# Kernel optimization log

Measured on AMD Instinct MI355X. Metric: run time of the kernel, lower is better.

Reference implementation:

```python
import jax, jax.numpy as jnp
import numpy as np

D = 64        # in_out_dim
M = 512       # hidden_dim
N = 4096      # batch
R = 10        # rank of quadratic term A (min(10, d+1))
ALPHA0 = 1.0  # alpha[0]
H = 1.0       # ResNet step h = 1/(nTh-1), nTh=2


def antideriv_tanh(x):
    # log(2*cosh(x)), numerically stable antiderivative of tanh
    ax = jnp.abs(x)
    return ax + jnp.log1p(jnp.exp(-2.0 * ax))


def setup_inputs() -> dict:
    key = jax.random.key(0)
    ks = jax.random.split(key, 10)
    f32 = jnp.float32
    return {
        "x":   jax.random.normal(ks[0], (N, D), f32),
        "t":   jax.random.uniform(ks[1], (), f32),
        "K0":  jax.random.normal(ks[2], (M, D + 1), f32) * (1.0 / np.sqrt(D + 1)),
        "b0":  jax.random.normal(ks[3], (M,), f32) * 0.1,
        "K1":  jax.random.normal(ks[4], (M, M), f32) * (1.0 / np.sqrt(M)),
        "b1":  jax.random.normal(ks[5], (M,), f32) * 0.1,
        "w":   jax.random.normal(ks[6], (M,), f32) * (1.0 / np.sqrt(M)),
        "A":   jax.random.normal(ks[7], (R, D + 1), f32) * (1.0 / np.sqrt(D + 1)),
        "c_w": jax.random.normal(ks[8], (D + 1,), f32) * 0.1,
        "c_b": jax.random.normal(ks[9], (), f32) * 0.1,
    }


def _tr_hess(s, K0, b0, K1, b1, w, A, c_w):
    # s: [N, d+1]; analytic gradient + Hessian trace of the OT-Flow potential.
    d = s.shape[1] - 1
    symA = A.T @ A                                   # [d+1, d+1]

    # forward through ResNet (nTh=2 -> one residual layer)
    opening = s @ K0.T + b0                          # [N, m]
    u0 = antideriv_tanh(opening)                     # [N, m]
    lin1 = u0 @ K1.T + b1                            # [N, m]

    tanh_open = jnp.tanh(opening)
    tanh_lin1 = jnp.tanh(lin1)

    # backward z-chain for the gradient
    z1 = w + H * (tanh_lin1 * w) @ K1                # [N, m]
    z0 = (tanh_open * z1) @ K0                       # [N, d+1]
    grad = z0 + s @ symA + c_w                       # [N, d+1]

    # trace of Hessian w.r.t. the first d coordinates
    Kopen = K0[:, :d]                                # [m, d]
    dt_open = 1.0 - tanh_open ** 2
    trH = (dt_open * z1) @ jnp.sum(Kopen ** 2, axis=1)          # [N]
    Jac = tanh_open[:, :, None] * Kopen[None]                    # [N, m, d]
    KJ = jnp.einsum('ij,njk->nik', K1, Jac)                      # [N, m, d]
    dt_lin1 = 1.0 - tanh_lin1 ** 2
    t1 = jnp.einsum('nj,njk->n', dt_lin1 * w, KJ ** 2)           # [N]
    trH = trH + H * t1 + jnp.trace(symA[:d, :d])
    return grad, trH


def reference(x, t, K0, b0, K1, b1, w, A, c_w, c_b):
    n = x.shape[0]
    s = jnp.concatenate([x, jnp.ones((n, 1), x.dtype) * t], axis=1)  # pad time
    gradPhi, trH = _tr_hess(s, K0, b0, K1, b1, w, A, c_w)
    dPhi_dx = gradPhi[:, :D]                         # [N, d]
    dPhi_dt = gradPhi[:, D:D + 1]                    # [N, 1]
    dz_dt = -(1.0 / ALPHA0) * dPhi_dx
    dlogp_dt = -(1.0 / ALPHA0) * trH[:, None]
    cost_L_dt = 0.5 * jnp.sum(dz_dt ** 2, axis=1, keepdims=True)
    cost_HJB_dt = jnp.abs(-dPhi_dt + ALPHA0 * cost_L_dt)
    return (dz_dt, dlogp_dt, cost_L_dt, cost_HJB_dt)
```

## Files before the change

### kernel.cpp

```cpp
#include <hip/hip_runtime.h>
#include <stdint.h>

#define D_  64
#define DP1 65
#define M_  512
#define N_  4096

typedef float f32x4 __attribute__((ext_vector_type(4)));
typedef _Float16 h8 __attribute__((ext_vector_type(8)));

__global__ void prepk(const float* __restrict__ A, const float* __restrict__ K0,
                      const float* __restrict__ K1, const float* __restrict__ x,
                      const float* __restrict__ tptr, const float* __restrict__ b0,
                      float* symA, float* sumK2,
                      _Float16* K1h, _Float16* K1Th, _Float16* K0Th,
                      _Float16* u0h, _Float16* ah, float* trH0){
  __shared__ float shm[2*64*66];
  int b = blockIdx.x;
  int t = threadIdx.x;
  if (b == 0){
    for (int idx = t; idx < DP1*DP1; idx += 256){
      int e = idx / DP1, d = idx % DP1;
      float s = 0.f;
      for (int r = 0; r < 10; ++r) s += A[r*DP1+e]*A[r*DP1+d];
      symA[idx] = s;
    }
    for (int m = t; m < M_; m += 256){
      float s = 0.f;
      for (int k = 0; k < D_; ++k){ float v = K0[m*DP1+k]; s += v*v; }
      sumK2[m] = s;
    }
  } else if (b < 65){
    int bb = b - 1;
    int r0 = (bb>>3)*64, c0 = (bb&7)*64;
    float* tile = shm;
    for (int it = 0; it < 16; ++it){
      int lin = it*256 + t;
      int r = lin >> 6, c = lin & 63;
      float v = K1[(r0+r)*M_ + c0+c];
      tile[r*65+c] = v;
      K1h[(r0+r)*M_ + c0+c] = (_Float16)v;
    }
    __syncthreads();
    for (int it = 0; it < 16; ++it){
      int lin = it*256 + t;
      int r = lin >> 6, c = lin & 63;
      K1Th[(c0+r)*M_ + (r0+c)] = (_Float16)tile[c*65+r];
    }
  } else if (b < 225){
    int idx = (b-65)*256 + t;
    if (idx < 80*M_){
      int d = idx / M_, i = idx % M_;
      float v = (d < DP1) ? K0[i*DP1 + d] : 0.f;
      K0Th[idx] = (_Float16)v;
    }
  } else {
    int bb = b - 225;
    int n0 = (bb & 63)*64, m0 = (bb >> 6)*64;
    float* sS = shm;
    float* sK = shm + 64*66;
    float tval = tptr[0];
    for (int it = 0; it < 17; ++it){
      int lin = it*256 + t;
      if (lin < 64*65){
        int r = lin/65, c = lin%65;
        sS[r*66+c] = (c < 64) ? x[(n0+r)*64 + c] : tval;
        sK[r*66+c] = K0[(m0+r)*DP1 + c];
      }
    }
    __syncthreads();
    int tn = (t>>4)*4, tm = (t&15)*4;
    float acc[4][4] = {};
    for (int e = 0; e < DP1; ++e){
      float sv[4], kv[4];
      for (int i=0;i<4;++i){ sv[i]=sS[(tn+i)*66+e]; kv[i]=sK[(tm+i)*66+e]; }
      for (int i=0;i<4;++i) for(int j=0;j<4;++j) acc[i][j] += sv[i]*kv[j];
    }
    for (int i=0;i<4;++i) for(int j=0;j<4;++j){
      int n = n0+tn+i, m = m0+tm+j;
      float o = acc[i][j] + b0[m];
      float a = tanhf(o);
      float ax = fabsf(o);
      float u0 = ax + log1pf(expf(-2.f*ax));
      u0h[n*M_+m] = (_Float16)u0;
      ah[n*M_+m]  = (_Float16)a;
    }
    if (m0 == 0 && t < 64) trH0[n0+t] = 0.f;
  }
}

template<int MODE>
__launch_bounds__(256, 4)
__global__ void gemm512(const _Float16* __restrict__ Ah, const _Float16* __restrict__ Wh,
                        const float* __restrict__ bias, const float* __restrict__ w,
                        const _Float16* __restrict__ ah, const float* __restrict__ sumK2,
                        _Float16* out0, _Float16* out1, float* trH0){
  int n0 = blockIdx.x*64, i0 = blockIdx.y*64;
  int t = threadIdx.x;
  int wv = t>>6, l = t&63;
  int r15 = l & 15;
  int krow = (l>>4)*8;
  const _Float16* abase = Ah + (size_t)(n0 + wv*16 + r15)*M_ + krow;
  const _Float16* wb0 = Wh + (size_t)(i0 +  0 + r15)*M_ + krow;
  const _Float16* wb1 = Wh + (size_t)(i0 + 16 + r15)*M_ + krow;
  const _Float16* wb2 = Wh + (size_t)(i0 + 32 + r15)*M_ + krow;
  const _Float16* wb3 = Wh + (size_t)(i0 + 48 + r15)*M_ + krow;
  f32x4 zero = {0.f,0.f,0.f,0.f};
  f32x4 acc[4]; for (int k=0;k<4;++k) acc[k]=zero;
  h8 af_c = *(const h8*)(abase);
  h8 bf_c0 = *(const h8*)(wb0);
  h8 bf_c1 = *(const h8*)(wb1);
  h8 bf_c2 = *(const h8*)(wb2);
  h8 bf_c3 = *(const h8*)(wb3);
  #pragma unroll
  for (int ii = 0; ii < 16; ++ii){
    const int j0 = ii*32;
    h8 af_n, bf_n0, bf_n1, bf_n2, bf_n3;
    if (ii < 15){
      af_n  = *(const h8*)(abase + j0 + 32);
      bf_n0 = *(const h8*)(wb0 + j0 + 32);
      bf_n1 = *(const h8*)(wb1 + j0 + 32);
      bf_n2 = *(const h8*)(wb2 + j0 + 32);
      bf_n3 = *(const h8*)(wb3 + j0 + 32);
    }
    acc[0] = __builtin_amdgcn_mfma_f32_16x16x32_f16(af_c, bf_c0, acc[0], 0, 0, 0);
    acc[1] = __builtin_amdgcn_mfma_f32_16x16x32_f16(af_c, bf_c1, acc[1], 0, 0, 0);
    acc[2] = __builtin_amdgcn_mfma_f32_16x16x32_f16(af_c, bf_c2, acc[2], 0, 0, 0);
    acc[3] = __builtin_amdgcn_mfma_f32_16x16x32_f16(af_c, bf_c3, acc[3], 0, 0, 0);
    if (ii < 15){
      af_c = af_n; bf_c0 = bf_n0; bf_c1 = bf_n1; bf_c2 = bf_n2; bf_c3 = bf_n3;
    }
  }
  if (MODE == 0){
    for (int kt=0;kt<4;++kt) for (int r=0;r<4;++r){
      int n = n0+wv*16+(l>>4)*4+r;
      int i = i0+kt*16+r15;
      float v = acc[kt][r] + bias[i];
      float tl = tanhf(v);
      out0[n*M_+i] = (_Float16)(tl*w[i]);
      out1[n*M_+i] = (_Float16)((1.f-tl*tl)*w[i]);
    }
  } else {
    for (int r=0;r<4;++r){
      int n = n0+wv*16+(l>>4)*4+r;
      float rowpart = 0.f;
      for (int kt=0;kt<4;++kt){
        int i = i0+kt*16+r15;
        float z1 = acc[kt][r] + w[i];
        float a = (float)ah[n*M_+i];
        out0[n*M_+i] = (_Float16)(a*z1);
        rowpart += (1.f-a*a)*z1*sumK2[i];
      }
      for (int m=1;m<16;m<<=1) rowpart += __shfl_xor(rowpart, m);
      if (r15==0) atomicAdd(&trH0[n], rowpart);
    }
  }
}

__launch_bounds__(256, 4)
__global__ void gemmz0(const _Float16* __restrict__ az1h, const _Float16* __restrict__ K0Th,
                       float* z0){
  int n0 = blockIdx.x*64;
  int t = threadIdx.x, wv = t>>6, l = t&63;
  int r15 = l & 15;
  int krow = (l>>4)*8;
  const _Float16* abase = az1h + (size_t)(n0 + wv*16 + r15)*M_ + krow;
  const _Float16* kb0 = K0Th + (size_t)( 0 + r15)*M_ + krow;
  const _Float16* kb1 = K0Th + (size_t)(16 + r15)*M_ + krow;
  const _Float16* kb2 = K0Th + (size_t)(32 + r15)*M_ + krow;
  const _Float16* kb3 = K0Th + (size_t)(48 + r15)*M_ + krow;
  const _Float16* kb4 = K0Th + (size_t)(64 + r15)*M_ + krow;
  f32x4 zero = {0.f,0.f,0.f,0.f};
  f32x4 acc[5]; for (int k=0;k<5;++k) acc[k]=zero;
  h8 af_c = *(const h8*)(abase);
  h8 b0c = *(const h8*)(kb0);
  h8 b1c = *(const h8*)(kb1);
  h8 b2c = *(const h8*)(kb2);
  h8 b3c = *(const h8*)(kb3);
  h8 b4c = *(const h8*)(kb4);
  #pragma unroll
  for (int ii = 0; ii < 16; ++ii){
    const int j0 = ii*32;
    h8 af_n, b0n, b1n, b2n, b3n, b4n;
    if (ii < 15){
      af_n = *(const h8*)(abase + j0 + 32);
      b0n = *(const h8*)(kb0 + j0 + 32);
      b1n = *(const h8*)(kb1 + j0 + 32);
      b2n = *(const h8*)(kb2 + j0 + 32);
      b3n = *(const h8*)(kb3 + j0 + 32);
      b4n = *(const h8*)(kb4 + j0 + 32);
    }
    acc[0] = __builtin_amdgcn_mfma_f32_16x16x32_f16(af_c, b0c, acc[0], 0, 0, 0);
    acc[1] = __builtin_amdgcn_mfma_f32_16x16x32_f16(af_c, b1c, acc[1], 0, 0, 0);
    acc[2] = __builtin_amdgcn_mfma_f32_16x16x32_f16(af_c, b2c, acc[2], 0, 0, 0);
    acc[3] = __builtin_amdgcn_mfma_f32_16x16x32_f16(af_c, b3c, acc[3], 0, 0, 0);
    acc[4] = __builtin_amdgcn_mfma_f32_16x16x32_f16(af_c, b4c, acc[4], 0, 0, 0);
    if (ii < 15){
      af_c = af_n; b0c = b0n; b1c = b1n; b2c = b2n; b3c = b3n; b4c = b4n;
    }
  }
  for (int dt=0; dt<5; ++dt) for (int r=0;r<4;++r){
    int n = n0+wv*16+(l>>4)*4+r;
    int d = dt*16+r15;
    z0[n*80+d] = acc[dt][r];
  }
}

__launch_bounds__(256, 2)
__global__ void kjk11(const _Float16* __restrict__ K1h, const _Float16* __restrict__ K0Th,
                      const _Float16* __restrict__ ah, const _Float16* __restrict__ ch,
                      float* trH0){
  __shared__ _Float16 sK1[64*512];
  __shared__ _Float16 sAv[8*512];
  int t = threadIdx.x;
  int n0 = blockIdx.x*8;
  int i0 = blockIdx.y*64;
  int wv = t>>6, l = t&63;
  int c15 = l & 15, g = l>>4;
  h8 kf[16];
  {
    const _Float16* kfp = K0Th + (size_t)(wv*16 + c15)*M_ + g*8;
    #pragma unroll
    for (int tt = 0; tt < 16; ++tt) kf[tt] = *(const h8*)(kfp + tt*32);
  }
  #pragma unroll
  for (int it = 0; it < 16; ++it){
    int r = it*4 + wv;
    const _Float16* src = K1h + (size_t)(i0 + r)*M_ + ((l ^ (r & 7))*8);
    __builtin_amdgcn_global_load_lds(
        (const __attribute__((address_space(1))) void*)src,
        (__attribute__((address_space(3))) void*)(&sK1[r*512]), 16, 0, 0);
  }
  #pragma unroll
  for (int it = 0; it < 2; ++it){
    int cc = it*256 + t;
    int s = cc >> 6, c = cc & 63;
    *(h8*)(&sAv[s*512 + c*8]) = *(const h8*)(ah + (size_t)(n0+s)*M_ + c*8);
  }
  __syncthreads();
  f32x4 zero = {0.f,0.f,0.f,0.f};
  f32x4 acc[4][8];
  #pragma unroll
  for (int tt=0;tt<4;++tt)
    #pragma unroll
    for (int s=0;s<8;++s) acc[tt][s]=zero;
  #pragma unroll
  for (int step = 0; step < 16; ++step){
    int p0 = (((step*4 + g) ^ (c15 & 7))*8);
    h8 bf0 = *(const h8*)(&sK1[(     c15)*512 + p0]);
    h8 bf1 = *(const h8*)(&sK1[(16 + c15)*512 + p0]);
    h8 bf2 = *(const h8*)(&sK1[(32 + c15)*512 + p0]);
    h8 bf3 = *(const h8*)(&sK1[(48 + c15)*512 + p0]);
    int aoff = step*32 + g*8;
    h8 k = kf[step];
    #pragma unroll
    for (int s = 0; s < 8; ++s){
      h8 av = *(const h8*)(&sAv[s*512 + aoff]);
      h8 ap = k*av;
      acc[0][s] = __builtin_amdgcn_mfma_f32_16x16x32_f16(ap, bf0, acc[0][s], 0, 0, 0);
      acc[1][s] = __builtin_amdgcn_mfma_f32_16x16x32_f16(ap, bf1, acc[1][s], 0, 0, 0);
      acc[2][s] = __builtin_amdgcn_mfma_f32_16x16x32_f16(ap, bf2, acc[2][s], 0, 0, 0);
      acc[3][s] = __builtin_amdgcn_mfma_f32_16x16x32_f16(ap, bf3, acc[3][s], 0, 0, 0);
    }
  }
  #pragma unroll
  for (int s = 0; s < 8; ++s){
    float part = 0.f;
    #pragma unroll
    for (int tt = 0; tt < 4; ++tt){
      float ci = (float)ch[(size_t)(n0+s)*M_ + i0 + tt*16 + c15];
      f32x4 a = acc[tt][s];
      part += ci*(a[0]*a[0] + a[1]*a[1] + a[2]*a[2] + a[3]*a[3]);
    }
    for (int m=32;m>=1;m>>=1) part += __shfl_xor(part, m);
    if (l == 0) atomicAdd(&trH0[n0+s], part);
  }
}

__global__ void finalk(const float* __restrict__ x, const float* __restrict__ tptr,
                       const float* __restrict__ symA, const float* __restrict__ c_w,
                       const float* __restrict__ z0, const float* __restrict__ trH0,
                       float* out){
  __shared__ float sA[DP1*DP1];
  int t = threadIdx.x;
  for (int i = t; i < DP1*DP1; i += 256) sA[i] = symA[i];
  __syncthreads();
  int wv = t>>6, l = t&63;
  int n = blockIdx.x*4 + wv;
  float tval = tptr[0];
  float sv = x[n*64 + l];
  float acc = z0[n*80 + l] + c_w[l];
  for (int e = 0; e < 64; ++e){
    float se = __shfl(sv, e);
    acc += se * sA[l*DP1 + e];
  }
  acc += tval * sA[l*DP1 + 64];
  float trd = sA[l*66];
  for (int m=32;m>=1;m>>=1) trd += __shfl_xor(trd, m);
  float g64 = sv * sA[64*DP1 + l];
  for (int m=32;m>=1;m>>=1) g64 += __shfl_xor(g64, m);
  g64 += tval*sA[64*DP1+64] + z0[n*80+64] + c_w[64];
  float dz = -acc;
  out[n*64 + l] = dz;
  float q = dz*dz;
  for (int m=32;m>=1;m>>=1) q += __shfl_xor(q, m);
  float costL = 0.5f*q;
  if (l == 0){
    out[N_*64 + n]        = -(trH0[n] + trd);
    out[N_*64 + N_ + n]   = costL;
    out[N_*64 + 2*N_ + n] = fabsf(-g64 + costL);
  }
}

extern "C" void kernel_launch(void* const* d_in, const int* in_sizes, int n_in,
                              void* d_out, int out_size, void* d_ws, size_t ws_size,
                              hipStream_t stream){
  const float* x   = (const float*)d_in[0];
  const float* tp  = (const float*)d_in[1];
  const float* K0  = (const float*)d_in[2];
  const float* b0  = (const float*)d_in[3];
  const float* K1  = (const float*)d_in[4];
  const float* b1  = (const float*)d_in[5];
  const float* w   = (const float*)d_in[6];
  const float* A   = (const float*)d_in[7];
  const float* c_w = (const float*)d_in[8];
  float* out = (float*)d_out;

  char* ws = (char*)d_ws;
  size_t off = 0;
  auto alloc = [&](size_t bytes)->void*{
    void* p = ws + off; off += bytes; off = (off + 255) & ~(size_t)255; return p;
  };
  _Float16* K1h   = (_Float16*)alloc(512*512*2);
  _Float16* K1Th  = (_Float16*)alloc(512*512*2);
  _Float16* K0Th  = (_Float16*)alloc(80*512*2);
  float* symA     = (float*)alloc(DP1*DP1*4);
  float* sumK2    = (float*)alloc(512*4);
  _Float16* u0h   = (_Float16*)alloc((size_t)N_*M_*2);
  _Float16* ah    = (_Float16*)alloc((size_t)N_*M_*2);
  _Float16* tl1wh = (_Float16*)alloc((size_t)N_*M_*2);
  _Float16* ch    = (_Float16*)alloc((size_t)N_*M_*2);
  _Float16* az1h  = (_Float16*)alloc((size_t)N_*M_*2);
  float* z0       = (float*)alloc((size_t)N_*80*4);
  float* trH0     = (float*)alloc(N_*4);

  prepk<<<737, 256, 0, stream>>>(A, K0, K1, x, tp, b0, symA, sumK2,
                                 K1h, K1Th, K0Th, u0h, ah, trH0);
  gemm512<0><<<dim3(N_/64, M_/64), 256, 0, stream>>>(u0h, K1h, b1, w, nullptr, nullptr,
                                                     tl1wh, ch, nullptr);
  gemm512<1><<<dim3(N_/64, M_/64), 256, 0, stream>>>(tl1wh, K1Th, nullptr, w, ah, sumK2,
                                                     az1h, nullptr, trH0);
  gemmz0<<<N_/64, 256, 0, stream>>>(az1h, K0Th, z0);
  kjk11<<<dim3(N_/8, 8), 256, 0, stream>>>(K1h, K0Th, ah, ch, trH0);
  finalk<<<N_/4, 256, 0, stream>>>(x, tp, symA, c_w, z0, trH0, out);
}
```

Before: 221.9 us.

## Split gemmz0 over K into four partial sums and raise MFMA priority in kjk

The z0 GEMM (N x 512 -> 80) now splits its K dimension across four blocks in a new grid y-dimension. Each block writes a partial result to its own slice of a buffer, and finalk adds the four slices. This takes the grid from 64 blocks to 256 so more CUs are busy, in exchange for extra partial-sum traffic and four loads per element in finalk. Separately, the kjk kernel raises wave priority around its MFMA inner loop with s_setprio, to favour issuing matrix instructions.

Measured after the change: 217.6 us. About the same (-1.9%).

```diff
diff --git a/kernel.cpp b/kernel.cpp
--- a/kernel.cpp
+++ b/kernel.cpp
@@ -159,11 +159,12 @@
 
 __launch_bounds__(256, 4)
 __global__ void gemmz0(const _Float16* __restrict__ az1h, const _Float16* __restrict__ K0Th,
-                       float* z0){
+                       float* z0p){
   int n0 = blockIdx.x*64;
+  int q  = blockIdx.y;
   int t = threadIdx.x, wv = t>>6, l = t&63;
   int r15 = l & 15;
-  int krow = (l>>4)*8;
+  int krow = q*128 + (l>>4)*8;
   const _Float16* abase = az1h + (size_t)(n0 + wv*16 + r15)*M_ + krow;
   const _Float16* kb0 = K0Th + (size_t)( 0 + r15)*M_ + krow;
   const _Float16* kb1 = K0Th + (size_t)(16 + r15)*M_ + krow;
@@ -172,42 +173,31 @@
   const _Float16* kb4 = K0Th + (size_t)(64 + r15)*M_ + krow;
   f32x4 zero = {0.f,0.f,0.f,0.f};
   f32x4 acc[5]; for (int k=0;k<5;++k) acc[k]=zero;
-  h8 af_c = *(const h8*)(abase);
-  h8 b0c = *(const h8*)(kb0);
-  h8 b1c = *(const h8*)(kb1);
-  h8 b2c = *(const h8*)(kb2);
-  h8 b3c = *(const h8*)(kb3);
-  h8 b4c = *(const h8*)(kb4);
-  #pragma unroll
-  for (int ii = 0; ii < 16; ++ii){
+  #pragma unroll
+  for (int ii = 0; ii < 4; ++ii){
     const int j0 = ii*32;
-    h8 af_n, b0n, b1n, b2n, b3n, b4n;
-    if (ii < 15){
-      af_n = *(const h8*)(abase + j0 + 32);
-      b0n = *(const h8*)(kb0 + j0 + 32);
-      b1n = *(const h8*)(kb1 + j0 + 32);
-      b2n = *(const h8*)(kb2 + j0 + 32);
-      b3n = *(const h8*)(kb3 + j0 + 32);
-      b4n = *(const h8*)(kb4 + j0 + 32);
-    }
-    acc[0] = __builtin_amdgcn_mfma_f32_16x16x32_f16(af_c, b0c, acc[0], 0, 0, 0);
-    acc[1] = __builtin_amdgcn_mfma_f32_16x16x32_f16(af_c, b1c, acc[1], 0, 0, 0);
-    acc[2] = __builtin_amdgcn_mfma_f32_16x16x32_f16(af_c, b2c, acc[2], 0, 0, 0);
-    acc[3] = __builtin_amdgcn_mfma_f32_16x16x32_f16(af_c, b3c, acc[3], 0, 0, 0);
-    acc[4] = __builtin_amdgcn_mfma_f32_16x16x32_f16(af_c, b4c, acc[4], 0, 0, 0);
-    if (ii < 15){
-      af_c = af_n; b0c = b0n; b1c = b1n; b2c = b2n; b3c = b3n; b4c = b4n;
-    }
-  }
+    h8 af = *(const h8*)(abase + j0);
+    h8 b0c = *(const h8*)(kb0 + j0);
+    h8 b1c = *(const h8*)(kb1 + j0);
+    h8 b2c = *(const h8*)(kb2 + j0);
+    h8 b3c = *(const h8*)(kb3 + j0);
+    h8 b4c = *(const h8*)(kb4 + j0);
+    acc[0] = __builtin_amdgcn_mfma_f32_16x16x32_f16(af, b0c, acc[0], 0, 0, 0);
+    acc[1] = __builtin_amdgcn_mfma_f32_16x16x32_f16(af, b1c, acc[1], 0, 0, 0);
+    acc[2] = __builtin_amdgcn_mfma_f32_16x16x32_f16(af, b2c, acc[2], 0, 0, 0);
+    acc[3] = __builtin_amdgcn_mfma_f32_16x16x32_f16(af, b3c, acc[3], 0, 0, 0);
+    acc[4] = __builtin_amdgcn_mfma_f32_16x16x32_f16(af, b4c, acc[4], 0, 0, 0);
+  }
+  float* zp = z0p + (size_t)q*N_*80;
   for (int dt=0; dt<5; ++dt) for (int r=0;r<4;++r){
     int n = n0+wv*16+(l>>4)*4+r;
     int d = dt*16+r15;
-    z0[n*80+d] = acc[dt][r];
+    zp[n*80+d] = acc[dt][r];
   }
 }
 
 __launch_bounds__(256, 2)
-__global__ void kjk11(const _Float16* __restrict__ K1h, const _Float16* __restrict__ K0Th,
+__global__ void kjk12(const _Float16* __restrict__ K1h, const _Float16* __restrict__ K0Th,
                       const _Float16* __restrict__ ah, const _Float16* __restrict__ ch,
                       float* trH0){
   __shared__ _Float16 sK1[64*512];
@@ -253,6 +243,7 @@
     h8 bf3 = *(const h8*)(&sK1[(48 + c15)*512 + p0]);
     int aoff = step*32 + g*8;
     h8 k = kf[step];
+    __builtin_amdgcn_s_setprio(1);
     #pragma unroll
     for (int s = 0; s < 8; ++s){
       h8 av = *(const h8*)(&sAv[s*512 + aoff]);
@@ -262,6 +253,7 @@
       acc[2][s] = __builtin_amdgcn_mfma_f32_16x16x32_f16(ap, bf2, acc[2][s], 0, 0, 0);
       acc[3][s] = __builtin_amdgcn_mfma_f32_16x16x32_f16(ap, bf3, acc[3][s], 0, 0, 0);
     }
+    __builtin_amdgcn_s_setprio(0);
   }
   #pragma unroll
   for (int s = 0; s < 8; ++s){
@@ -279,7 +271,7 @@
 
 __global__ void finalk(const float* __restrict__ x, const float* __restrict__ tptr,
                        const float* __restrict__ symA, const float* __restrict__ c_w,
-                       const float* __restrict__ z0, const float* __restrict__ trH0,
+                       const float* __restrict__ z0p, const float* __restrict__ trH0,
                        float* out){
   __shared__ float sA[DP1*DP1];
   int t = threadIdx.x;
@@ -289,7 +281,11 @@
   int n = blockIdx.x*4 + wv;
   float tval = tptr[0];
   float sv = x[n*64 + l];
-  float acc = z0[n*80 + l] + c_w[l];
+  float z0l = z0p[(size_t)0*N_*80 + n*80 + l] + z0p[(size_t)1*N_*80 + n*80 + l]
+            + z0p[(size_t)2*N_*80 + n*80 + l] + z0p[(size_t)3*N_*80 + n*80 + l];
+  float z0t = z0p[(size_t)0*N_*80 + n*80 + 64] + z0p[(size_t)1*N_*80 + n*80 + 64]
+            + z0p[(size_t)2*N_*80 + n*80 + 64] + z0p[(size_t)3*N_*80 + n*80 + 64];
+  float acc = z0l + c_w[l];
   for (int e = 0; e < 64; ++e){
     float se = __shfl(sv, e);
     acc += se * sA[l*DP1 + e];
@@ -299,7 +295,7 @@
   for (int m=32;m>=1;m>>=1) trd += __shfl_xor(trd, m);
   float g64 = sv * sA[64*DP1 + l];
   for (int m=32;m>=1;m>>=1) g64 += __shfl_xor(g64, m);
-  g64 += tval*sA[64*DP1+64] + z0[n*80+64] + c_w[64];
+  g64 += tval*sA[64*DP1+64] + z0t + c_w[64];
   float dz = -acc;
   out[n*64 + l] = dz;
   float q = dz*dz;
@@ -341,7 +337,7 @@
   _Float16* tl1wh = (_Float16*)alloc((size_t)N_*M_*2);
   _Float16* ch    = (_Float16*)alloc((size_t)N_*M_*2);
   _Float16* az1h  = (_Float16*)alloc((size_t)N_*M_*2);
-  float* z0       = (float*)alloc((size_t)N_*80*4);
+  float* z0p      = (float*)alloc((size_t)4*N_*80*4);
   float* trH0     = (float*)alloc(N_*4);
 
   prepk<<<737, 256, 0, stream>>>(A, K0, K1, x, tp, b0, symA, sumK2,
@@ -350,7 +346,7 @@
                                                      tl1wh, ch, nullptr);
   gemm512<1><<<dim3(N_/64, M_/64), 256, 0, stream>>>(tl1wh, K1Th, nullptr, w, ah, sumK2,
                                                      az1h, nullptr, trH0);
-  gemmz0<<<N_/64, 256, 0, stream>>>(az1h, K0Th, z0);
-  kjk11<<<dim3(N_/8, 8), 256, 0, stream>>>(K1h, K0Th, ah, ch, trH0);
-  finalk<<<N_/4, 256, 0, stream>>>(x, tp, symA, c_w, z0, trH0, out);
-}
+  gemmz0<<<dim3(N_/64, 4), 256, 0, stream>>>(az1h, K0Th, z0p);
+  kjk12<<<dim3(N_/8, 8), 256, 0, stream>>>(K1h, K0Th, ah, ch, trH0);
+  finalk<<<N_/4, 256, 0, stream>>>(x, tp, symA, c_w, z0p, trH0, out);
+}
```
